# Kernel tuning notes

Measured on AMD Instinct MI355X. Metric: run time of the kernel, lower is better.

Reference implementation:

```python
import jax, jax.numpy as jnp
import numpy as np

B, N, C, K1, K2, TD = 4, 4096, 128, 16, 8, 64
CIN = 2 * (3 + C)  # 262


def setup_inputs() -> dict:
    key = jax.random.key(0)
    ks = jax.random.split(key, 8)
    s = 0.05
    feature = jax.random.normal(ks[0], (B, C, N), jnp.float32)
    xyz = jax.random.normal(ks[1], (B, 3, N), jnp.float32)
    wq = jax.random.normal(ks[2], (TD, CIN), jnp.float32) * s
    wk = jax.random.normal(ks[3], (TD, CIN), jnp.float32) * s
    wv = jax.random.normal(ks[4], (TD, CIN), jnp.float32) * s
    w1 = jax.random.normal(ks[5], (C, TD), jnp.float32) * s
    bq = jnp.zeros((TD,), jnp.float32)
    bk = jnp.zeros((TD,), jnp.float32)
    bv = jnp.zeros((TD,), jnp.float32)
    b1 = jnp.zeros((C,), jnp.float32)
    return {"feature": feature, "xyz": xyz, "wq": wq, "bq": bq,
            "wk": wk, "bk": bk, "wv": wv, "bv": bv, "w1": w1, "b1": b1}


def _group(x, ind):
    # x: [B, Cx, N], ind: [B, N, K] -> [B, Cx, K, N]; g[b,c,k,n] = x[b,c,ind[b,n,k]]
    g = jnp.take_along_axis(x[:, :, None, :], ind[:, None, :, :], axis=3)  # [B,Cx,N,K]
    return g.transpose(0, 1, 3, 2)


def reference(feature, xyz, wq, bq, wk, bk, wv, bv, w1, b1):
    # --- KNN (self-included then dropped), idx[b,n,k] = k-th nearest of point n ---
    sq = jnp.sum(xyz * xyz, axis=1)                                   # [B,N]
    dist = sq[:, :, None] + sq[:, None, :] - 2.0 * jnp.einsum('bdn,bdm->bnm', xyz, xyz)
    _, idx = jax.lax.top_k(-dist, K1 + 1)                             # [B,N,17]
    idx = idx[:, :, 1:]                                               # drop self -> [B,N,16]
    idx1 = idx[:, :, :K2]                                             # [B,N,8]

    gxyz = _group(xyz, idx)        # [B,3,16,N]
    gxyz1 = _group(xyz, idx1)      # [B,3,8,N]
    gfea = _group(feature, idx)    # [B,C,16,N]
    gfea1 = _group(feature, idx1)  # [B,C,8,N]

    rel_xyz = gxyz - xyz[:, :, None, :]
    rel_xyz1 = gxyz1 - xyz[:, :, None, :]
    rel_fea = gfea - feature[:, :, None, :]
    rel_fea1 = gfea1 - feature[:, :, None, :]

    def relpos(rx, rf, K):
        return jnp.concatenate([
            rx,
            jnp.broadcast_to(xyz[:, :, None, :], (B, 3, K, N)),
            rf,
            jnp.broadcast_to(feature[:, :, None, :], (B, C, K, N)),
        ], axis=1)  # [B,262,K,N]

    rel_pos = relpos(rel_xyz, rel_fea, K1)     # [B,262,16,N]
    rel_pos1 = relpos(rel_xyz1, rel_fea1, K2)  # [B,262,8,N]

    # 1x1 Conv2d projections
    q = jnp.einsum('oc,bckn->bokn', wq, rel_pos1) + bq[None, :, None, None]  # [B,64,8,N]
    k = jnp.einsum('oc,bckn->bokn', wk, rel_pos) + bk[None, :, None, None]   # [B,64,16,N]
    v = jnp.einsum('oc,bckn->bokn', wv, rel_pos) + bv[None, :, None, None]   # [B,64,16,N]

    attn = jnp.einsum('bmnf,bmjf->bnjf', q, k)   # [B,8,16,N]
    attn = jax.nn.softmax(attn, axis=-2)         # softmax over j (16 neighbors)
    res = jnp.einsum('bnjf,bmjf->bmf', attn, v)  # [B,64,N]

    out = jnp.einsum('om,bmf->bof', w1, res) + b1[None, :, None]  # Conv1d 64->128
    return out + feature
```

## Files before the change

### kernel.cpp

```cpp
#include <hip/hip_runtime.h>

#define NN 4096
#define CCH 128

typedef float f2 __attribute__((ext_vector_type(2)));
typedef float f4 __attribute__((ext_vector_type(4)));

__device__ __forceinline__ void cmpex(float& x, float& y) {
  float mn = fminf(x, y);
  y = fmaxf(x, y);
  x = mn;
}

template <int N>
__device__ __forceinline__ void bitonic_merge(float* s) {
#pragma unroll
  for (int jm = N / 2; jm > 0; jm >>= 1)
#pragma unroll
    for (int i = 0; i < N; ++i)
      if ((i & jm) == 0) cmpex(s[i], s[i + jm]);
}

__device__ __forceinline__ void merge44(float* a, const float* b) {
  float m0 = fminf(a[0], b[3]), m1 = fminf(a[1], b[2]);
  float m2 = fminf(a[2], b[1]), m3 = fminf(a[3], b[0]);
  cmpex(m0, m2); cmpex(m1, m3); cmpex(m0, m1); cmpex(m2, m3);
  a[0] = m0; a[1] = m1; a[2] = m2; a[3] = m3;
}

__global__ __launch_bounds__(256) void transpose_w(
    const float* __restrict__ wq, const float* __restrict__ wk, const float* __restrict__ wv,
    const float* __restrict__ w1, const float* __restrict__ xyz,
    float* __restrict__ wTq, float* __restrict__ wTk, float* __restrict__ wTv,
    float* __restrict__ w1T, float* __restrict__ wPack, float4* __restrict__ pts4,
    float* __restrict__ pp) {
  int t = blockIdx.x * 256 + threadIdx.x;
  if (t < 64 * 262) {
    int o = t / 262, c = t - o * 262;
    wTq[c * 64 + o] = wq[t];
    wTk[c * 64 + o] = wk[t];
    wTv[c * 64 + o] = wv[t];
  }
  if (t < 128 * 64) {
    int r = t >> 6, c2 = t & 63;
    w1T[c2 * 128 + r] = w1[t];
  }
  if (t < 49152) {
    int c  = t & 3;
    int o  = (t >> 2) & 63;
    int ph = (t >> 8) & 1;
    int t2 = t >> 9;
    int mm = t2 % 3;
    int t3 = t2 / 3;
    int ct = t3 & 15;
    int half = t3 >> 4;
    const float* wsrc = (mm == 0) ? wq : ((mm == 1) ? wk : wv);
    int isT = c & 1;
    int rr  = 2 * ph + (c >> 1);
    int col = (isT ? 134 : 6) + 4 * (half * 16 + ct) + rr;
    wPack[t] = wsrc[o * 262 + col];
  }
  if (t < 4 * NN) {
    int bb = t >> 12, i = t & 4095;
    const float* xb = xyz + (size_t)bb * 3 * NN;
    float x = xb[i], y = xb[NN + i], z = xb[2 * NN + i];
    float w = x * x + y * y + z * z;
    pts4[t] = make_float4(x, y, z, w);
    float* pb = pp + ((size_t)bb * 2048 + (i >> 1)) * 8 + (i & 1);
    pb[0] = x; pb[2] = y; pb[4] = z; pb[6] = w;
  }
}

__global__ __launch_bounds__(1024, 4) void knn_half(const float4* __restrict__ pts4,
                                                    const float* __restrict__ pp,
                                                    unsigned long long* __restrict__ keys_ws) {
  __shared__ float bufA[64 * 64];
  __shared__ float bufB[64 * 64];
  __shared__ unsigned long long hits[32 * 65];
  __shared__ int cnt[64];
  const int b  = blockIdx.x >> 7;
  const int g  = (blockIdx.x >> 1) & 63;
  const int h  = blockIdx.x & 1;
  const int n0 = g << 6;
  const int ql = threadIdx.x & 63;
  const int ch = __builtin_amdgcn_readfirstlane(threadIdx.x >> 6);
  if (threadIdx.x < 64) cnt[threadIdx.x] = 0;
  const int q = n0 + ql;
  const float4* pb4 = pts4 + ((size_t)b << 12);
  const float4 me = pb4[q];
  const f2 mex = {me.x, me.x}, mey = {me.y, me.y}, mez = {me.z, me.z}, mew = {me.w, me.w};
  const f2 mneg2 = {-2.0f, -2.0f};
  const float* ppb = pp + ((size_t)b << 14);
  const int m0 = (h << 11) + (ch << 7);
  const bool ovl = (((h << 4) + ch) == (n0 >> 7));
  float t0[4], t1[4], t2[4], t3[4];
#pragma unroll
  for (int u = 0; u < 4; ++u) { t0[u] = 3.0e38f; t1[u] = 3.0e38f; t2[u] = 3.0e38f; t3[u] = 3.0e38f; }
#pragma unroll 2
  for (int mb = m0; mb < m0 + 128; mb += 8) {
    const f4* pg4 = reinterpret_cast<const f4*>(ppb + (size_t)mb * 4);
    f2 d2[4];
#pragma unroll
    for (int u = 0; u < 4; ++u) {
      f4 A = pg4[2 * u], B = pg4[2 * u + 1];
      f2 X = A.xy, Y = A.zw, Z = B.xy, W = B.zw;
      f2 dot = X * mex + Y * mey + Z * mez;
      d2[u] = dot * mneg2 + (W + mew);
    }
    if (ovl) {
#pragma unroll
      for (int u = 0; u < 4; ++u) {
        d2[u].x = (mb + 2 * u     == q) ? 3.0e38f : d2[u].x;
        d2[u].y = (mb + 2 * u + 1 == q) ? 3.0e38f : d2[u].y;
      }
    }
#pragma unroll
    for (int u = 0; u < 4; ++u) {
      float* bd = (u == 0) ? t0 : (u == 1) ? t1 : (u == 2) ? t2 : t3;
      float dx = d2[u].x, dy = d2[u].y;
      bd[3] = __builtin_amdgcn_fmed3f(dx, bd[2], bd[3]);
      bd[2] = __builtin_amdgcn_fmed3f(dx, bd[1], bd[2]);
      bd[1] = __builtin_amdgcn_fmed3f(dx, bd[0], bd[1]);
      bd[0] = fminf(bd[0], dx);
      bd[3] = __builtin_amdgcn_fmed3f(dy, bd[2], bd[3]);
      bd[2] = __builtin_amdgcn_fmed3f(dy, bd[1], bd[2]);
      bd[1] = __builtin_amdgcn_fmed3f(dy, bd[0], bd[1]);
      bd[0] = fminf(bd[0], dy);
    }
  }
  merge44(t0, t1); merge44(t2, t3); merge44(t0, t2);
  {
    const int r0 = (ch * 4) * 64 + ql;
    bufA[r0] = t0[0]; bufA[r0 + 64] = t0[1]; bufA[r0 + 128] = t0[2]; bufA[r0 + 192] = t0[3];
  }
  __syncthreads();
  if (ch < 8) {
    const int base = 8 * ch;
    float s[8];
#pragma unroll
    for (int i = 0; i < 4; ++i) s[i] = bufA[(base + i) * 64 + ql];
#pragma unroll
    for (int i = 0; i < 4; ++i) s[4 + i] = bufA[(base + 7 - i) * 64 + ql];
    bitonic_merge<8>(s);
#pragma unroll
    for (int i = 0; i < 8; ++i) bufB[(base + i) * 64 + ql] = s[i];
  }
  __syncthreads();
  if (ch < 4) {
    const int base = 16 * ch;
    float s[16];
#pragma unroll
    for (int i = 0; i < 8; ++i) s[i] = bufB[(base + i) * 64 + ql];
#pragma unroll
    for (int i = 0; i < 8; ++i) s[8 + i] = bufB[(base + 15 - i) * 64 + ql];
    bitonic_merge<16>(s);
#pragma unroll
    for (int i = 0; i < 16; ++i) bufA[(base + i) * 64 + ql] = s[i];
  }
  __syncthreads();
  if (ch < 2) {
    const int base = 32 * ch;
    float l[16];
#pragma unroll
    for (int i = 0; i < 16; ++i)
      l[i] = fminf(bufA[(base + i) * 64 + ql], bufA[(base + 31 - i) * 64 + ql]);
    bitonic_merge<16>(l);
#pragma unroll
    for (int i = 0; i < 16; ++i) bufB[(16 * ch + i) * 64 + ql] = l[i];
  }
  __syncthreads();
  if (ch == 0) {
    float m[16];
#pragma unroll
    for (int i = 0; i < 16; ++i)
      m[i] = fminf(bufB[i * 64 + ql], bufB[(31 - i) * 64 + ql]);
    float t = m[0];
#pragma unroll
    for (int i = 1; i < 16; ++i) t = fmaxf(t, m[i]);
    bufA[15 * 64 + ql] = t;
  }
  __syncthreads();
  const float tau = bufA[15 * 64 + ql];
#pragma unroll 2
  for (int mb = m0; mb < m0 + 128; mb += 8) {
    const f4* pg4 = reinterpret_cast<const f4*>(ppb + (size_t)mb * 4);
#pragma unroll
    for (int u = 0; u < 4; ++u) {
      f4 A = pg4[2 * u], B = pg4[2 * u + 1];
      f2 X = A.xy, Y = A.zw, Z = B.xy, W = B.zw;
      f2 dot = X * mex + Y * mey + Z * mez;
      f2 d2 = dot * mneg2 + (W + mew);
      if (fminf(d2.x, d2.y) <= tau) {
        if (d2.x <= tau && (mb + 2 * u) != q) {
          int pos = atomicAdd(&cnt[ql], 1);
          if (pos < 32) {
            unsigned int f = __float_as_uint(d2.x);
            f ^= (f >> 31) ? 0xFFFFFFFFu : 0x80000000u;
            hits[pos * 65 + ql] = ((unsigned long long)f << 32) | (unsigned int)(mb + 2 * u);
          }
        }
        if (d2.y <= tau && (mb + 2 * u + 1) != q) {
          int pos = atomicAdd(&cnt[ql], 1);
          if (pos < 32) {
            unsigned int f = __float_as_uint(d2.y);
            f ^= (f >> 31) ? 0xFFFFFFFFu : 0x80000000u;
            hits[pos * 65 + ql] = ((unsigned long long)f << 32) | (unsigned int)(mb + 2 * u + 1);
          }
        }
      }
    }
  }
  __syncthreads();
  const int l5 = threadIdx.x & 31;
#pragma unroll
  for (int t = 0; t < 2; ++t) {
    const int qq = (t * 1024 + (int)threadIdx.x) >> 5;
    int nv = cnt[qq]; nv = nv > 32 ? 32 : nv;
    unsigned long long key = (l5 < nv) ? hits[l5 * 65 + qq] : ~0ULL;
#pragma unroll
    for (int k = 2; k <= 32; k <<= 1) {
#pragma unroll
      for (int jm = k >> 1; jm > 0; jm >>= 1) {
        unsigned long long o2 = __shfl_xor(key, jm, 32);
        bool asc = ((l5 & k) == 0);
        bool lower = ((l5 & jm) == 0);
        unsigned long long mn = key < o2 ? key : o2;
        unsigned long long mx = key < o2 ? o2 : key;
        key = (lower == asc) ? mn : mx;
      }
    }
    if (l5 < 16) {
      const size_t gq = (size_t)((b << 12) + n0 + qq);
      keys_ws[((size_t)h << 18) + gq * 16 + l5] = key;
    }
  }
}

__global__ __launch_bounds__(512) void proj_kernel(
    const float* __restrict__ feature, const float4* __restrict__ pts4,
    const float* __restrict__ wTq, const float* __restrict__ wTk, const float* __restrict__ wTv,
    const float* __restrict__ wPack,
    const float* __restrict__ bq, const float* __restrict__ bk, const float* __restrict__ bv,
    float* __restrict__ uqA, float* __restrict__ cq,
    float2* __restrict__ ukv,
    float* __restrict__ ck, float* __restrict__ cv) {
  __shared__ float fl[64][128];
  __shared__ float4 wl[8 * 3 * 2 * 64];
  const int p0 = blockIdx.x << 6;
  const int b  = p0 >> 12;
  const int n0 = p0 & 4095;
  {
    const int i  = threadIdx.x & 63;
    const int c0 = threadIdx.x >> 6;
    const float* fb = feature + (size_t)b * CCH * NN + n0 + i;
    for (int cc = c0; cc < CCH; cc += 8) fl[i][cc] = fb[(size_t)cc * NN];
  }
  const int o  = threadIdx.x & 63;
  const int pg = threadIdx.x >> 6;
  const float4* wp = reinterpret_cast<const float4*>(wPack);
  f2 acc[3][8];
#pragma unroll
  for (int mm = 0; mm < 3; ++mm)
#pragma unroll
    for (int s = 0; s < 8; ++s) acc[mm][s] = (f2){0.f, 0.f};

  for (int qtr = 0; qtr < 4; ++qtr) {
    __syncthreads();
    for (int d4 = threadIdx.x; d4 < 3072; d4 += 512)
      wl[d4] = wp[qtr * 3072 + d4];
    __syncthreads();
#pragma unroll
    for (int ct = 0; ct < 8; ++ct) {
      float4 wA[3], wB[3];
#pragma unroll
      for (int mm = 0; mm < 3; ++mm) {
        wA[mm] = wl[((ct * 3 + mm) * 2 + 0) * 64 + o];
        wB[mm] = wl[((ct * 3 + mm) * 2 + 1) * 64 + o];
      }
      const int cglob = qtr * 8 + ct;
#pragma unroll
      for (int s = 0; s < 8; ++s) {
        const float4 f4w = *reinterpret_cast<const float4*>(&fl[pg * 8 + s][4 * cglob]);
        const f2 sx = {f4w.x, f4w.x}, sy = {f4w.y, f4w.y}, sz = {f4w.z, f4w.z}, sw = {f4w.w, f4w.w};
#pragma unroll
        for (int mm = 0; mm < 3; ++mm) {
          const f2* a2 = reinterpret_cast<const f2*>(&wA[mm]);
          const f2* b2 = reinterpret_cast<const f2*>(&wB[mm]);
          f2 a = acc[mm][s];
          a += sx * a2[0];
          a += sy * a2[1];
          a += sz * b2[0];
          a += sw * b2[1];
          acc[mm][s] = a;
        }
      }
    }
  }
  float wxu[3][3], wxt[3][3];
#pragma unroll
  for (int dd = 0; dd < 3; ++dd) {
    wxu[0][dd] = wTq[dd * 64 + o]; wxt[0][dd] = wTq[(3 + dd) * 64 + o];
    wxu[1][dd] = wTk[dd * 64 + o]; wxt[1][dd] = wTk[(3 + dd) * 64 + o];
    wxu[2][dd] = wTv[dd * 64 + o]; wxt[2][dd] = wTv[(3 + dd) * 64 + o];
  }
  const float bo0 = bq[o], bo1 = bk[o], bo2 = bv[o];
  const float4* pt = pts4 + ((size_t)b << 12) + n0;
#pragma unroll
  for (int s = 0; s < 8; ++s) {
    const int p = pg * 8 + s;
    const float4 P = pt[p];
    const float x = P.x, y = P.y, z = P.z;
    const size_t gp = ((size_t)(p0 + p)) * 64 + o;
    float uu, tt;
    uu = acc[0][s].x + wxu[0][0] * x + wxu[0][1] * y + wxu[0][2] * z;
    tt = acc[0][s].y + wxt[0][0] * x + wxt[0][1] * y + wxt[0][2] * z;
    uqA[gp] = uu; cq[gp] = tt + bo0 - uu;
    const float uk_ = acc[1][s].x + wxu[1][0] * x + wxu[1][1] * y + wxu[1][2] * z;
    tt = acc[1][s].y + wxt[1][0] * x + wxt[1][1] * y + wxt[1][2] * z;
    ck[gp] = tt + bo1 - uk_;
    const float uv_ = acc[2][s].x + wxu[2][0] * x + wxu[2][1] * y + wxu[2][2] * z;
    tt = acc[2][s].y + wxt[2][0] * x + wxt[2][1] * y + wxt[2][2] * z;
    cv[gp] = tt + bo2 - uv_;
    ukv[gp] = make_float2(uk_, uv_);
  }
}

__global__ __launch_bounds__(256) void attn_core(
    const unsigned long long* __restrict__ keys_ws,
    const float* __restrict__ uqA, const float* __restrict__ cq,
    const float2* __restrict__ ukv,
    const float* __restrict__ ck, const float* __restrict__ cv,
    float* __restrict__ res_ws) {
  __shared__ float kq[4][24][68];
  const int slot = threadIdx.x >> 6;
  const int o    = threadIdx.x & 63;
  const int p = (blockIdx.x << 2) + slot;
  const int b = p >> 12;
  const int l5 = o & 31;
  unsigned long long key =
      (l5 < 16) ? keys_ws[(size_t)p * 16 + l5]
                : keys_ws[((size_t)1 << 18) + (size_t)p * 16 + (31 - l5)];
#pragma unroll
  for (int jm = 16; jm > 0; jm >>= 1) {
    unsigned long long o2 = __shfl_xor(key, jm, 32);
    bool lower = ((l5 & jm) == 0);
    unsigned long long mn = key < o2 ? key : o2;
    unsigned long long mx = key < o2 ? o2 : key;
    key = lower ? mn : mx;
  }
  const int kidx = (int)(key & 0xFFFFFFFFu);
  const size_t pb = (size_t)p * 64 + o;
  const float cqo = cq[pb], cko = ck[pb], cvo = cv[pb];
  const int rowbase = (b << 12) * 64;
  float v[16];
#pragma unroll
  for (int j = 0; j < 16; ++j) {
    int nb = __shfl(kidx, j);
    int row = rowbase + nb * 64 + o;
    float2 kv = ukv[row];
    kq[slot][j][o] = kv.x + cko;
    v[j] = kv.y + cvo;
    if (j < 8) kq[slot][16 + j][o] = uqA[row] + cqo;
  }
  const int i  = o >> 3;
  const int jj = o & 7;
  const float* qrow = &kq[slot][16 + i][0];
  const float* k0r  = &kq[slot][jj][0];
  const float* k1r  = &kq[slot][8 + jj][0];
  float s0 = 0.f, s1 = 0.f;
#pragma unroll
  for (int t = 0; t < 16; ++t) {
    float4 q4 = *reinterpret_cast<const float4*>(qrow + 4 * t);
    float4 a4 = *reinterpret_cast<const float4*>(k0r + 4 * t);
    float4 c4 = *reinterpret_cast<const float4*>(k1r + 4 * t);
    s0 += q4.x * a4.x + q4.y * a4.y + q4.z * a4.z + q4.w * a4.w;
    s1 += q4.x * c4.x + q4.y * c4.y + q4.z * c4.z + q4.w * c4.w;
  }
  float mx = fmaxf(s0, s1);
  mx = fmaxf(mx, __shfl_xor(mx, 1));
  mx = fmaxf(mx, __shfl_xor(mx, 2));
  mx = fmaxf(mx, __shfl_xor(mx, 4));
  float e0 = __expf(s0 - mx), e1 = __expf(s1 - mx);
  float den = e0 + e1;
  den += __shfl_xor(den, 1);
  den += __shfl_xor(den, 2);
  den += __shfl_xor(den, 4);
  const float inv = 1.0f / den;
  float w0 = e0 * inv, w1s = e1 * inv;
  w0 += __shfl_xor(w0, 8);   w1s += __shfl_xor(w1s, 8);
  w0 += __shfl_xor(w0, 16);  w1s += __shfl_xor(w1s, 16);
  w0 += __shfl_xor(w0, 32);  w1s += __shfl_xor(w1s, 32);
  float res = 0.f;
#pragma unroll
  for (int j = 0; j < 8; ++j) {
    res += __shfl(w0, j)  * v[j];
    res += __shfl(w1s, j) * v[j + 8];
  }
  res_ws[pb] = res;
}

__global__ __launch_bounds__(512) void out_kernel(
    const float* __restrict__ feature, const float* __restrict__ res,
    const float* __restrict__ w1T, const float* __restrict__ b1,
    float* __restrict__ out) {
  __shared__ float rT[64][66];
  const int p0 = blockIdx.x << 6;
  const int b  = p0 >> 12;
  const int n0 = p0 & 4095;
  {
    const int o = threadIdx.x & 63;
    for (int pp = threadIdx.x >> 6; pp < 64; pp += 8)
      rT[o][pp] = res[(size_t)(p0 + pp) * 64 + o];
  }
  __syncthreads();
  const int n = threadIdx.x & 63;
  const int c0 = (threadIdx.x >> 6) * 16;
  float acc[16];
#pragma unroll
  for (int cc = 0; cc < 16; ++cc) acc[cc] = b1[c0 + cc];
  for (int o = 0; o < 64; ++o) {
    const float rr = rT[o][n];
    const float* wrow = &w1T[o * 128 + c0];
#pragma unroll
    for (int cc = 0; cc < 16; ++cc) acc[cc] += wrow[cc] * rr;
  }
#pragma unroll
  for (int cc = 0; cc < 16; ++cc) {
    const size_t gi = ((size_t)(b * 128 + c0 + cc) << 12) + n0 + n;
    out[gi] = acc[cc] + feature[gi];
  }
}

extern "C" void kernel_launch(void* const* d_in, const int* in_sizes, int n_in,
                              void* d_out, int out_size, void* d_ws, size_t ws_size,
                              hipStream_t stream) {
  const float* feature = (const float*)d_in[0];
  const float* xyz     = (const float*)d_in[1];
  const float* wq      = (const float*)d_in[2];
  const float* bq      = (const float*)d_in[3];
  const float* wk      = (const float*)d_in[4];
  const float* bk      = (const float*)d_in[5];
  const float* wv      = (const float*)d_in[6];
  const float* bv      = (const float*)d_in[7];
  const float* w1      = (const float*)d_in[8];
  const float* b1      = (const float*)d_in[9];
  float* out = (float*)d_out;

  char* ws = (char*)d_ws;
  float4* pts4 = (float4*)(ws + (1u << 20));
  float*  pp   = (float*)(ws + (1u << 20) + 262144);
  float*  uqA  = (float*)(ws + (2u << 20));
  float*  cq   = (float*)(ws + (6u << 20));
  float*  ck   = (float*)(ws + (10u << 20));
  float*  cv   = (float*)(ws + (14u << 20));
  float2* ukv  = (float2*)(ws + (18u << 20));
  float*  res  = (float*)(ws + (26u << 20));
  float*  wTq  = (float*)(ws + (30u << 20));
  float*  wTk  = wTq + 262 * 64;
  float*  wTv  = wTk + 262 * 64;
  float*  w1T  = wTv + 262 * 64;
  float*  wPk  = w1T + 128 * 64;
  unsigned long long* keys = (unsigned long long*)(ws + (31u << 20));

  transpose_w<<<192, 256, 0, stream>>>(wq, wk, wv, w1, xyz, wTq, wTk, wTv, w1T, wPk, pts4, pp);
  knn_half<<<512, 1024, 0, stream>>>(pts4, pp, keys);
  proj_kernel<<<256, 512, 0, stream>>>(feature, pts4, wTq, wTk, wTv, wPk, bq, bk, bv,
                                       uqA, cq, ukv, ck, cv);
  attn_core<<<4096, 256, 0, stream>>>(keys, uqA, cq, ukv, ck, cv, res);
  out_kernel<<<256, 512, 0, stream>>>(feature, res, w1T, b1, out);
}
```

Baseline: 196.3 us.

## Split KNN candidate range into quarters with smaller blocks and merge four partial lists

The KNN kernel now splits each query's 4096 candidates across four 512-thread blocks instead of two 1024-thread blocks, giving 1024 blocks with less shared memory each and one fewer reduction stage. The attention kernel now loads four partial top-16 key lists and merges them with an extra bitonic merge round plus a cross-half shuffle. This aims to raise occupancy and shorten the KNN tail. The cost is a larger keys workspace and more merge work in attn_core.

```diff
diff --git a/kernel.cpp b/kernel.cpp
--- a/kernel.cpp
+++ b/kernel.cpp
@@ -71,16 +71,17 @@
   }
 }
 
-__global__ __launch_bounds__(1024, 4) void knn_half(const float4* __restrict__ pts4,
-                                                    const float* __restrict__ pp,
-                                                    unsigned long long* __restrict__ keys_ws) {
-  __shared__ float bufA[64 * 64];
-  __shared__ float bufB[64 * 64];
-  __shared__ unsigned long long hits[32 * 65];
+__global__ __launch_bounds__(512, 8) void knn_quarter(const float4* __restrict__ pts4,
+                                                      const float* __restrict__ pp,
+                                                      unsigned long long* __restrict__ keys_ws) {
+  __shared__ float bufA[32 * 64];
+  __shared__ unsigned long long ubuf[32 * 65];
   __shared__ int cnt[64];
-  const int b  = blockIdx.x >> 7;
-  const int g  = (blockIdx.x >> 1) & 63;
-  const int h  = blockIdx.x & 1;
+  float* bufB = (float*)ubuf;
+  unsigned long long* hits = ubuf;
+  const int b  = blockIdx.x >> 8;
+  const int g  = (blockIdx.x >> 2) & 63;
+  const int qd = blockIdx.x & 3;
   const int n0 = g << 6;
   const int ql = threadIdx.x & 63;
   const int ch = __builtin_amdgcn_readfirstlane(threadIdx.x >> 6);
@@ -91,8 +92,8 @@
   const f2 mex = {me.x, me.x}, mey = {me.y, me.y}, mez = {me.z, me.z}, mew = {me.w, me.w};
   const f2 mneg2 = {-2.0f, -2.0f};
   const float* ppb = pp + ((size_t)b << 14);
-  const int m0 = (h << 11) + (ch << 7);
-  const bool ovl = (((h << 4) + ch) == (n0 >> 7));
+  const int m0 = (qd << 10) + (ch << 7);
+  const bool ovl = ((m0 >> 7) == (n0 >> 7));
   float t0[4], t1[4], t2[4], t3[4];
 #pragma unroll
   for (int u = 0; u < 4; ++u) { t0[u] = 3.0e38f; t1[u] = 3.0e38f; t2[u] = 3.0e38f; t3[u] = 3.0e38f; }
@@ -134,7 +135,7 @@
     bufA[r0] = t0[0]; bufA[r0 + 64] = t0[1]; bufA[r0 + 128] = t0[2]; bufA[r0 + 192] = t0[3];
   }
   __syncthreads();
-  if (ch < 8) {
+  if (ch < 4) {
     const int base = 8 * ch;
     float s[8];
 #pragma unroll
@@ -146,7 +147,7 @@
     for (int i = 0; i < 8; ++i) bufB[(base + i) * 64 + ql] = s[i];
   }
   __syncthreads();
-  if (ch < 4) {
+  if (ch < 2) {
     const int base = 16 * ch;
     float s[16];
 #pragma unroll
@@ -158,22 +159,11 @@
     for (int i = 0; i < 16; ++i) bufA[(base + i) * 64 + ql] = s[i];
   }
   __syncthreads();
-  if (ch < 2) {
-    const int base = 32 * ch;
-    float l[16];
-#pragma unroll
-    for (int i = 0; i < 16; ++i)
-      l[i] = fminf(bufA[(base + i) * 64 + ql], bufA[(base + 31 - i) * 64 + ql]);
-    bitonic_merge<16>(l);
-#pragma unroll
-    for (int i = 0; i < 16; ++i) bufB[(16 * ch + i) * 64 + ql] = l[i];
-  }
-  __syncthreads();
   if (ch == 0) {
     float m[16];
 #pragma unroll
     for (int i = 0; i < 16; ++i)
-      m[i] = fminf(bufB[i * 64 + ql], bufB[(31 - i) * 64 + ql]);
+      m[i] = fminf(bufA[i * 64 + ql], bufA[(31 - i) * 64 + ql]);
     float t = m[0];
 #pragma unroll
     for (int i = 1; i < 16; ++i) t = fmaxf(t, m[i]);
@@ -213,8 +203,8 @@
   __syncthreads();
   const int l5 = threadIdx.x & 31;
 #pragma unroll
-  for (int t = 0; t < 2; ++t) {
-    const int qq = (t * 1024 + (int)threadIdx.x) >> 5;
+  for (int t = 0; t < 4; ++t) {
+    const int qq = (t * 512 + (int)threadIdx.x) >> 5;
     int nv = cnt[qq]; nv = nv > 32 ? 32 : nv;
     unsigned long long key = (l5 < nv) ? hits[l5 * 65 + qq] : ~0ULL;
 #pragma unroll
@@ -231,7 +221,7 @@
     }
     if (l5 < 16) {
       const size_t gq = (size_t)((b << 12) + n0 + qq);
-      keys_ws[((size_t)h << 18) + gq * 16 + l5] = key;
+      keys_ws[((size_t)qd << 18) + gq * 16 + l5] = key;
     }
   }
 }
@@ -337,9 +327,24 @@
   const int p = (blockIdx.x << 2) + slot;
   const int b = p >> 12;
   const int l5 = o & 31;
-  unsigned long long key =
-      (l5 < 16) ? keys_ws[(size_t)p * 16 + l5]
-                : keys_ws[((size_t)1 << 18) + (size_t)p * 16 + (31 - l5)];
+  {
+  }
+  const int grp  = o >> 5;
+  const int qsel = grp * 2 + (l5 < 16 ? 0 : 1);
+  const int idx  = (l5 < 16) ? l5 : (31 - l5);
+  unsigned long long key = keys_ws[((size_t)qsel << 18) + (size_t)p * 16 + idx];
+#pragma unroll
+  for (int jm = 16; jm > 0; jm >>= 1) {
+    unsigned long long o2 = __shfl_xor(key, jm, 32);
+    bool lower = ((l5 & jm) == 0);
+    unsigned long long mn = key < o2 ? key : o2;
+    unsigned long long mx = key < o2 ? o2 : key;
+    key = lower ? mn : mx;
+  }
+  {
+    unsigned long long other = __shfl(key, 63 - o, 64);
+    if (o & 16) key = other;
+  }
 #pragma unroll
   for (int jm = 16; jm > 0; jm >>= 1) {
     unsigned long long o2 = __shfl_xor(key, jm, 32);
@@ -463,7 +468,7 @@
   unsigned long long* keys = (unsigned long long*)(ws + (31u << 20));
 
   transpose_w<<<192, 256, 0, stream>>>(wq, wk, wv, w1, xyz, wTq, wTk, wTv, w1T, wPk, pts4, pp);
-  knn_half<<<512, 1024, 0, stream>>>(pts4, pp, keys);
+  knn_quarter<<<1024, 512, 0, stream>>>(pts4, pp, keys);
   proj_kernel<<<256, 512, 0, stream>>>(feature, pts4, wTq, wTk, wTv, wPk, bq, bk, bv,
                                        uqA, cq, ukv, ck, cv);
   attn_core<<<4096, 256, 0, stream>>>(keys, uqA, cq, ukv, ck, cv, res);
```

Measured after the change: 205.9 us. 1.05x slower.
